# Kernel optimization log

Hardware: AMD Instinct MI355X
Metric: run time of the kernel (lower is better)

## Reference

```python
import jax, jax.numpy as jnp
import numpy as np

C = 64          # residual channels
N_LAYERS = 30
MAX_STEPS = 200
SQRT2 = 2.0 ** 0.5


def _conv1d(x, W, b, dilation=1, pad=0):
    # x: [B, Cin, T], W: [Cout, Cin, K], b: [Cout]
    y = jax.lax.conv_general_dilated(
        x, W, window_strides=(1,), padding=[(pad, pad)],
        rhs_dilation=(dilation,), dimension_numbers=('NCH', 'OIH', 'NCH'))
    return y + b[None, :, None]


def _silu(x):
    return x * jax.nn.sigmoid(x)


def _emb_table():
    steps = jnp.arange(MAX_STEPS, dtype=jnp.float32)[:, None]      # [200,1]
    dims = jnp.arange(64, dtype=jnp.float32)[None, :]              # [1,64]
    t = steps * 10.0 ** (dims * 4.0 / 63.0)                        # [200,64]
    return jnp.concatenate([jnp.sin(t), jnp.cos(t)], axis=1)       # [200,128]


def setup_inputs() -> dict:
    key = jax.random.key(0)
    ks = jax.random.split(key, 20)
    B, T = 4, 16384
    f32 = jnp.float32
    inp = {
        'audio': jax.random.normal(ks[0], (B, 1, T), dtype=f32),
        'diffusion_step': jax.random.randint(ks[1], (B,), 0, MAX_STEPS),
        # input projection Conv1d(1, 64, 1)
        'in_W': jax.random.normal(ks[2], (C, 1, 1), f32) * 1.0,
        'in_b': jax.random.normal(ks[3], (C,), f32) * 0.01,
        # diffusion embedding MLP 128->512->512
        'p1_W': jax.random.normal(ks[4], (512, 128), f32) * (1.0 / np.sqrt(128)),
        'p1_b': jnp.zeros((512,), f32),
        'p2_W': jax.random.normal(ks[5], (512, 512), f32) * (1.0 / np.sqrt(512)),
        'p2_b': jnp.zeros((512,), f32),
        # per-layer params (stacked over 30 layers)
        'dw_W': jax.random.normal(ks[6], (N_LAYERS, 2 * C, C, 3), f32) * (1.0 / np.sqrt(3 * C)),
        'dw_b': jnp.zeros((N_LAYERS, 2 * C), f32),
        'dp_W': jax.random.normal(ks[7], (N_LAYERS, C, 512), f32) * (1.0 / np.sqrt(512)),
        'dp_b': jnp.zeros((N_LAYERS, C), f32),
        'op_W': jax.random.normal(ks[8], (N_LAYERS, 2 * C, C, 1), f32) * (1.0 / np.sqrt(C)),
        'op_b': jnp.zeros((N_LAYERS, 2 * C), f32),
        # skip projection Conv1d(64,64,1)
        'sk_W': jax.random.normal(ks[9], (C, C, 1), f32) * (1.0 / np.sqrt(C)),
        'sk_b': jnp.zeros((C,), f32),
        # output projection Conv1d(64,1,1), weight zero-init like original
        'out_W': jnp.zeros((1, C, 1), f32),
        'out_b': jax.random.normal(ks[10], (1,), f32) * 0.01,
    }
    return inp


def reference(audio, diffusion_step, in_W, in_b, p1_W, p1_b, p2_W, p2_b,
              dw_W, dw_b, dp_W, dp_b, op_W, op_b, sk_W, sk_b, out_W, out_b):
    x = jax.nn.relu(_conv1d(audio, in_W, in_b))                    # [B,64,T]
    # diffusion embedding
    t = _emb_table()[diffusion_step]                               # [B,128]
    t = _silu(t @ p1_W.T + p1_b)                                   # [B,512]
    t = _silu(t @ p2_W.T + p2_b)                                   # [B,512]
    skip = None
    for i in range(N_LAYERS):
        d = 2 ** (i % 10)
        cond = (t @ dp_W[i].T + dp_b[i])[:, :, None]               # [B,64,1]
        y = _conv1d(x + cond, dw_W[i], dw_b[i], dilation=d, pad=d) # [B,128,T]
        gate, filt = y[:, :C], y[:, C:]
        y = jax.nn.sigmoid(gate) * jnp.tanh(filt)                  # [B,64,T]
        y = _conv1d(y, op_W[i], op_b[i])                           # [B,128,T]
        residual, sk = y[:, :C], y[:, C:]
        x = (x + residual) / SQRT2
        skip = sk if skip is None else skip + sk
    x = skip / np.sqrt(float(N_LAYERS)).astype(np.float32)
    x = jax.nn.relu(_conv1d(x, sk_W, sk_b))
    return _conv1d(x, out_W, out_b)                                # [B,1,T]
```

## Files before the change

### kernel.cpp

```cpp
#include <hip/hip_runtime.h>
#include <math.h>

#define C 64
#define NL 30
#define T 16384
#define B 4

typedef __bf16 bf16_t;
typedef __bf16 bf16x8 __attribute__((ext_vector_type(8)));
typedef __bf16 bf16x4 __attribute__((ext_vector_type(4)));
typedef float f32x4 __attribute__((ext_vector_type(4)));

typedef const __attribute__((address_space(1))) unsigned int glb_u32;
typedef __attribute__((address_space(3))) unsigned int lds_u32;

constexpr float INV_SQRT2   = 0.70710678118654752440f;
constexpr float INV_SQRT_NL = 0.18257418583505537115f;

__device__ __forceinline__ float fsig(float x) {
    return __builtin_amdgcn_rcpf(1.f + __builtin_amdgcn_exp2f(-1.44269504089f * x));
}
__device__ __forceinline__ float ftanh(float x) {
    return fmaf(2.f, __builtin_amdgcn_rcpf(1.f + __builtin_amdgcn_exp2f(-2.88539008178f * x)), -1.f);
}
__device__ __forceinline__ int swz(int off) { return off ^ ((off >> 3) & 0x70); }

__global__ void pack_weights(const float* __restrict__ dw_W,
                             const float* __restrict__ op_W,
                             const float* __restrict__ sk_W,
                             bf16_t* __restrict__ convpk,
                             bf16_t* __restrict__ oppk,
                             bf16_t* __restrict__ skpk) {
    int idx = blockIdx.x * 256 + threadIdx.x;
    const int ndw = NL * 128 * 192;
    const int nop = NL * 128 * 64;
    if (idx < ndw) {
        int k = idx % 192; int r = idx / 192;
        int oc = r % 128;  int l = r / 128;
        int tap = k >> 6, ic = k & 63;
        convpk[idx] = (bf16_t)dw_W[((l * 128 + oc) * 64 + ic) * 3 + tap];
    } else if (idx < ndw + nop) {
        oppk[idx - ndw] = (bf16_t)op_W[idx - ndw];
    } else if (idx < ndw + nop + 4096) {
        int j = idx - ndw - nop;
        skpk[j] = (bf16_t)(sk_W[j] * INV_SQRT_NL);
    }
}

__global__ void cond_embp1(const int* __restrict__ step,
                           const float* __restrict__ p1_W, const float* __restrict__ p1_b,
                           float* __restrict__ h1out) {
    __shared__ float e[128];
    __shared__ float red[256];
    int b = blockIdx.x, blk = blockIdx.y, tid = threadIdx.x;
    int s = step[b];
    if (tid < 128) {
        int d = tid & 63;
        float tf = (float)s * powf(10.f, (float)d * 4.f / 63.f);
        double td = (double)tf;
        e[tid] = (tid < 64) ? (float)sin(td) : (float)cos(td);
    }
    __syncthreads();
    int ol = tid >> 2, q = tid & 3;
    int o = blk * 64 + ol;
    const float4* wr = (const float4*)(p1_W + o * 128 + q * 32);
    const float4* ev = (const float4*)(e + q * 32);
    float a = 0.f;
    #pragma unroll
    for (int j = 0; j < 8; ++j) {
        float4 wv = wr[j]; float4 xv = ev[j];
        a = fmaf(wv.x, xv.x, a); a = fmaf(wv.y, xv.y, a);
        a = fmaf(wv.z, xv.z, a); a = fmaf(wv.w, xv.w, a);
    }
    red[tid] = a;
    __syncthreads();
    if (q == 0) {
        float v = red[tid] + red[tid + 1] + red[tid + 2] + red[tid + 3] + p1_b[o];
        h1out[b * 512 + o] = v / (1.f + expf(-v));
    }
}

__global__ void cond_p2(const float* __restrict__ h1,
                        const float* __restrict__ p2_W, const float* __restrict__ p2_b,
                        float* __restrict__ h2out) {
    __shared__ float red[256];
    int b = blockIdx.x, blk = blockIdx.y, tid = threadIdx.x;
    int ol = tid >> 2, q = tid & 3;
    int o = blk * 64 + ol;
    const float4* wr = (const float4*)(p2_W + o * 512 + q * 128);
    const float4* hv = (const float4*)(h1 + b * 512 + q * 128);
    float a = 0.f;
    #pragma unroll 8
    for (int j = 0; j < 32; ++j) {
        float4 wv = wr[j]; float4 xv = hv[j];
        a = fmaf(wv.x, xv.x, a); a = fmaf(wv.y, xv.y, a);
        a = fmaf(wv.z, xv.z, a); a = fmaf(wv.w, xv.w, a);
    }
    red[tid] = a;
    __syncthreads();
    if (q == 0) {
        float v = red[tid] + red[tid + 1] + red[tid + 2] + red[tid + 3] + p2_b[o];
        h2out[b * 512 + o] = v / (1.f + expf(-v));
    }
}

__global__ void cond_stage2b(const float* __restrict__ h2,
                             const float* __restrict__ dp_W, const float* __restrict__ dp_b,
                             const bf16_t* __restrict__ convpk,
                             const float* __restrict__ dw_b,
                             float* __restrict__ bias2) {
    __shared__ float red[256];
    __shared__ float cond_s[64];
    int l = blockIdx.x, b = blockIdx.y;
    int tid = threadIdx.x;
    {
        int o = tid >> 2, q = tid & 3;
        const float4* wr = (const float4*)(dp_W + ((size_t)l * C + o) * 512 + q * 128);
        const float4* h = (const float4*)(h2 + b * 512 + q * 128);
        float a = 0.f;
        #pragma unroll 8
        for (int j = 0; j < 32; ++j) {
            float4 wv = wr[j]; float4 hv = h[j];
            a = fmaf(wv.x, hv.x, a); a = fmaf(wv.y, hv.y, a);
            a = fmaf(wv.z, hv.z, a); a = fmaf(wv.w, hv.w, a);
        }
        red[tid] = a;
        __syncthreads();
        if (q == 0)
            cond_s[o] = red[tid] + red[tid + 1] + red[tid + 2] + red[tid + 3] + dp_b[l * C + o];
    }
    __syncthreads();
    int oc = tid & 127, kh = tid >> 7;
    const bf16_t* wr = convpk + ((size_t)l * 128 + oc) * 192 + kh * 96;
    float a = kh ? 0.f : dw_b[l * 128 + oc];
    #pragma unroll
    for (int j = 0; j < 96; ++j)
        a = fmaf((float)wr[j], cond_s[(kh * 96 + j) & 63], a);
    __syncthreads();
    red[tid] = a;
    __syncthreads();
    if (tid < 128)
        bias2[(l * B + b) * 128 + tid] = red[tid] + red[tid + 128];
}

__global__ void in_conv(const float* __restrict__ audio,
                        const float* __restrict__ in_W, const float* __restrict__ in_b,
                        bf16_t* __restrict__ x) {
    int idx = blockIdx.x * 256 + threadIdx.x;
    int cb = idx & 7;
    int t = (idx >> 3) & (T - 1);
    int b = idx >> 17;
    float av = audio[b * T + t];
    bf16x8 o;
    #pragma unroll
    for (int j = 0; j < 8; ++j) {
        int c = cb * 8 + j;
        o[j] = (bf16_t)fmaxf(fmaf(in_W[c], av, in_b[c]), 0.f);
    }
    *(bf16x8*)(x + ((size_t)b * T + t) * 64 + cb * 8) = o;
}

__global__ __launch_bounds__(256) void layer_kernel(
    const bf16_t* __restrict__ x_in, bf16_t* __restrict__ x_out, bf16_t* __restrict__ skip,
    const bf16_t* __restrict__ convpk, const bf16_t* __restrict__ oppk,
    const float* __restrict__ bias2, const float* __restrict__ op_b,
    const bf16_t* __restrict__ zpage,
    int layer, int dil, int first)
{
    __shared__ uint4 smem_u[4096];
    char* sm = (char*)smem_u;

    int tid = threadIdx.x;
    int w = __builtin_amdgcn_readfirstlane(tid >> 6);
    int l = tid & 63;
    int lr = l & 15;
    int g = l >> 4;
    int b = blockIdx.y;
    int tbase = blockIdx.x * 128;
    const bf16_t* xb = x_in + (size_t)b * T * 64;
    const bool m1 = (dil <= 32);

#define STAGE_M1(Sbase, t0s, R)                                              \
    _Pragma("unroll")                                                        \
    for (int r = 0; r < (R); ++r) {                                          \
        int q = r * 4096 + tid * 16;                                         \
        int row = q >> 7, c16 = (q >> 4) & 7;                                \
        int ts = (t0s) - dil + row;                                          \
        int c16s = c16 ^ (row & 7);                                          \
        const bf16_t* src = ((unsigned)ts < (unsigned)T)                     \
            ? xb + (size_t)ts * 64 + c16s * 8 : zpage + c16s * 8;            \
        __builtin_amdgcn_global_load_lds((glb_u32*)src,                      \
            (lds_u32*)(sm + (Sbase) + r * 4096 + w * 1024), 16, 0, 0);       \
    }
#define STAGE_M3(Sbase, t0s)                                                 \
    _Pragma("unroll")                                                        \
    for (int it = 0; it < 6; ++it) {                                         \
        int qq = it * 256 + tid;                                             \
        int slice = qq >> 9, row = (qq >> 3) & 63, c16 = qq & 7;             \
        int ts = (t0s) + row + (slice - 1) * dil;                            \
        int c16s = c16 ^ (row & 7);                                          \
        const bf16_t* src = ((unsigned)ts < (unsigned)T)                     \
            ? xb + (size_t)ts * 64 + c16s * 8 : zpage + c16s * 8;            \
        __builtin_amdgcn_global_load_lds((glb_u32*)src,                      \
            (lds_u32*)(sm + (Sbase) + it * 4096 + w * 1024), 16, 0, 0);      \
    }

    if (dil <= 16) {
        STAGE_M1(0, tbase, 3)
        STAGE_M1(24576, tbase + 64, 3)
        asm volatile("s_waitcnt vmcnt(3)" ::: "memory");
    } else if (dil == 32) {
        STAGE_M1(0, tbase, 4)
        STAGE_M1(24576, tbase + 64, 4)
        asm volatile("s_waitcnt vmcnt(4)" ::: "memory");
    } else {
        STAGE_M3(0, tbase)
        STAGE_M3(24576, tbase + 64)
        asm volatile("s_waitcnt vmcnt(6)" ::: "memory");
    }
    __builtin_amdgcn_s_barrier();
    __builtin_amdgcn_sched_barrier(0);
    asm volatile("" ::: "memory");

    bf16x8 cA[2][6];
    const bf16_t* cw = convpk + (size_t)layer * 128 * 192;
    #pragma unroll
    for (int mf = 0; mf < 2; ++mf)
        #pragma unroll
        for (int kf = 0; kf < 6; ++kf)
            cA[mf][kf] = *(const bf16x8*)(cw + (mf * 64 + w * 16 + lr) * 192 + kf * 32 + g * 8);
    bf16x8 oA[2][2];
    const bf16_t* ow = oppk + (size_t)layer * 128 * 64;
    #pragma unroll
    for (int mf = 0; mf < 2; ++mf)
        #pragma unroll
        for (int kf = 0; kf < 2; ++kf)
            oA[mf][kf] = *(const bf16x8*)(ow + (mf * 64 + w * 16 + lr) * 64 + kf * 32 + g * 8);
    f32x4 bC[2], bO[2];
    const float* b2 = bias2 + (layer * B + b) * 128;
    const float* ob = op_b + layer * 2 * C;
    #pragma unroll
    for (int mf = 0; mf < 2; ++mf)
        #pragma unroll
        for (int r = 0; r < 4; ++r) {
            bC[mf][r] = b2[mf * 64 + w * 16 + g * 4 + r];
            bO[mf][r] = ob[mf * 64 + w * 16 + g * 4 + r];
        }

    size_t bb = (size_t)b * T * 64;
    int tapstride = m1 ? dil * 128 : 8192;
    int t1off = m1 ? dil * 128 : 8192;

    for (int st = 0; st < 2; ++st) {
        int Sb = st * 24576;
        int zb = 49152 + st * 8192;
        int t0 = tbase + st * 64;

        f32x4 acc[2][4];
        #pragma unroll
        for (int mf = 0; mf < 2; ++mf)
            #pragma unroll
            for (int nf = 0; nf < 4; ++nf) acc[mf][nf] = bC[mf];
        #pragma unroll
        for (int kf = 0; kf < 6; ++kf) {
            int tap = kf >> 1;
            int kc = (kf & 1) * 32;
            bf16x8 Bf[4];
            #pragma unroll
            for (int nf = 0; nf < 4; ++nf) {
                int off = Sb + tap * tapstride + (nf * 16 + lr) * 128 + (kc + g * 8) * 2;
                Bf[nf] = *(const bf16x8*)(sm + swz(off));
            }
            #pragma unroll
            for (int mf = 0; mf < 2; ++mf)
                #pragma unroll
                for (int nf = 0; nf < 4; ++nf)
                    acc[mf][nf] = __builtin_amdgcn_mfma_f32_16x16x32_bf16(
                        cA[mf][kf], Bf[nf], acc[mf][nf], 0, 0, 0);
        }

        #pragma unroll
        for (int nf = 0; nf < 4; ++nf) {
            union { bf16_t hh[4]; uint2 u; } zp;
            #pragma unroll
            for (int r = 0; r < 4; ++r)
                zp.hh[r] = (bf16_t)(fsig(acc[0][nf][r]) * ftanh(acc[1][nf][r]));
            int off = zb + (nf * 16 + lr) * 128 + (w * 16 + g * 4) * 2;
            *(uint2*)(sm + swz(off)) = zp.u;
        }
        __syncthreads();

        f32x4 acc2[2][4];
        #pragma unroll
        for (int mf = 0; mf < 2; ++mf)
            #pragma unroll
            for (int nf = 0; nf < 4; ++nf) acc2[mf][nf] = bO[mf];
        #pragma unroll
        for (int kf = 0; kf < 2; ++kf) {
            bf16x8 Zf[4];
            #pragma unroll
            for (int nf = 0; nf < 4; ++nf) {
                int off = zb + (nf * 16 + lr) * 128 + (kf * 32 + g * 8) * 2;
                Zf[nf] = *(const bf16x8*)(sm + swz(off));
            }
            #pragma unroll
            for (int mf = 0; mf < 2; ++mf)
                #pragma unroll
                for (int nf = 0; nf < 4; ++nf)
                    acc2[mf][nf] = __builtin_amdgcn_mfma_f32_16x16x32_bf16(
                        oA[mf][kf], Zf[nf], acc2[mf][nf], 0, 0, 0);
        }

        #pragma unroll
        for (int nf = 0; nf < 4; ++nf) {
            int t = t0 + nf * 16 + lr;
            int c0 = w * 16 + g * 4;
            int xoff = Sb + t1off + (nf * 16 + lr) * 128 + c0 * 2;
            bf16x4 xv = *(const bf16x4*)(sm + swz(xoff));
            bf16x4 ro, so;
            bf16_t* sp = skip + bb + (size_t)t * 64 + c0;
            if (first) {
                #pragma unroll
                for (int r = 0; r < 4; ++r) {
                    ro[r] = (bf16_t)(((float)xv[r] + acc2[0][nf][r]) * INV_SQRT2);
                    so[r] = (bf16_t)acc2[1][nf][r];
                }
            } else {
                bf16x4 sv = *(const bf16x4*)sp;
                #pragma unroll
                for (int r = 0; r < 4; ++r) {
                    ro[r] = (bf16_t)(((float)xv[r] + acc2[0][nf][r]) * INV_SQRT2);
                    so[r] = (bf16_t)((float)sv[r] + acc2[1][nf][r]);
                }
            }
            *(bf16x4*)(x_out + bb + (size_t)t * 64 + c0) = ro;
            *(bf16x4*)sp = so;
        }
    }
#undef STAGE_M1
#undef STAGE_M3
}

__global__ __launch_bounds__(256) void final_kernel(
    const bf16_t* __restrict__ skip, const bf16_t* __restrict__ skpk,
    const float* __restrict__ sk_b,
    const float* __restrict__ out_W, const float* __restrict__ out_b,
    float* __restrict__ out)
{
    __shared__ uint4 tile_u[512];
    __shared__ float part[16][66];
    unsigned char* sm = (unsigned char*)tile_u;
    int tid = threadIdx.x;
    int w = __builtin_amdgcn_readfirstlane(tid >> 6);
    int l = tid & 63, lr = l & 15, g = l >> 4;
    int b = blockIdx.y, t0 = blockIdx.x * 64;
    const bf16_t* sb = skip + (size_t)b * T * 64;

    #pragma unroll
    for (int it = 0; it < 2; ++it) {
        int q = it * 256 + tid;
        int row = q >> 3, c16 = q & 7;
        uint4 val = *(const uint4*)(sb + (size_t)(t0 + row) * 64 + c16 * 8);
        *(uint4*)(sm + swz(row * 128 + c16 * 16)) = val;
    }

    bf16x8 aS[2];
    #pragma unroll
    for (int kf = 0; kf < 2; ++kf)
        aS[kf] = *(const bf16x8*)(skpk + (w * 16 + lr) * 64 + kf * 32 + g * 8);
    f32x4 acc[4];
    #pragma unroll
    for (int nf = 0; nf < 4; ++nf)
        #pragma unroll
        for (int r = 0; r < 4; ++r) acc[nf][r] = sk_b[w * 16 + g * 4 + r];
    __syncthreads();

    #pragma unroll
    for (int kf = 0; kf < 2; ++kf) {
        bf16x8 Bf[4];
        #pragma unroll
        for (int nf = 0; nf < 4; ++nf) {
            int off = (nf * 16 + lr) * 128 + (kf * 32 + g * 8) * 2;
            Bf[nf] = *(const bf16x8*)(sm + swz(off));
        }
        #pragma unroll
        for (int nf = 0; nf < 4; ++nf)
            acc[nf] = __builtin_amdgcn_mfma_f32_16x16x32_bf16(aS[kf], Bf[nf], acc[nf], 0, 0, 0);
    }

    #pragma unroll
    for (int nf = 0; nf < 4; ++nf) {
        float o = 0.f;
        #pragma unroll
        for (int r = 0; r < 4; ++r)
            o = fmaf(out_W[w * 16 + g * 4 + r], fmaxf(acc[nf][r], 0.f), o);
        part[w * 4 + g][nf * 16 + lr] = o;
    }
    __syncthreads();
    if (tid < 64) {
        float o = out_b[0];
        #pragma unroll
        for (int j = 0; j < 16; ++j) o += part[j][tid];
        out[(size_t)b * T + t0 + tid] = o;
    }
}

extern "C" void kernel_launch(void* const* d_in, const int* in_sizes, int n_in,
                              void* d_out, int out_size, void* d_ws, size_t ws_size,
                              hipStream_t stream) {
    const float* audio = (const float*)d_in[0];
    const int*   dstep = (const int*)d_in[1];
    const float* in_W  = (const float*)d_in[2];
    const float* in_b  = (const float*)d_in[3];
    const float* p1_W  = (const float*)d_in[4];
    const float* p1_b  = (const float*)d_in[5];
    const float* p2_W  = (const float*)d_in[6];
    const float* p2_b  = (const float*)d_in[7];
    const float* dw_W  = (const float*)d_in[8];
    const float* dw_b  = (const float*)d_in[9];
    const float* dp_W  = (const float*)d_in[10];
    const float* dp_b  = (const float*)d_in[11];
    const float* op_W  = (const float*)d_in[12];
    const float* op_b  = (const float*)d_in[13];
    const float* sk_W  = (const float*)d_in[14];
    const float* sk_b  = (const float*)d_in[15];
    const float* out_W = (const float*)d_in[16];
    const float* out_b = (const float*)d_in[17];

    float* ws = (float*)d_ws;
    const size_t NXE = (size_t)B * T * 64;
    float* h1    = ws;
    float* h2    = h1 + B * 512;
    float* bias2 = h2 + B * 512;
    float* zpg   = bias2 + NL * B * 128;
    bf16_t* xA   = (bf16_t*)(zpg + 128);
    bf16_t* xB   = xA + NXE;
    bf16_t* skip = xB + NXE;
    bf16_t* convpk = skip + NXE;
    bf16_t* oppk   = convpk + (size_t)NL * 128 * 192;
    bf16_t* skpk   = oppk + (size_t)NL * 128 * 64;

    hipMemsetAsync(zpg, 0, 512, stream);
    hipLaunchKernelGGL(pack_weights, dim3(3856), dim3(256), 0, stream,
                       dw_W, op_W, sk_W, convpk, oppk, skpk);
    hipLaunchKernelGGL(cond_embp1, dim3(B, 8), dim3(256), 0, stream,
                       dstep, p1_W, p1_b, h1);
    hipLaunchKernelGGL(cond_p2, dim3(B, 8), dim3(256), 0, stream,
                       h1, p2_W, p2_b, h2);
    hipLaunchKernelGGL(cond_stage2b, dim3(NL, B), dim3(256), 0, stream,
                       h2, dp_W, dp_b, convpk, dw_b, bias2);
    hipLaunchKernelGGL(in_conv, dim3(B * T * 8 / 256), dim3(256), 0, stream,
                       audio, in_W, in_b, xA);
    for (int i = 0; i < NL; ++i) {
        bf16_t* xin  = (i & 1) ? xB : xA;
        bf16_t* xout = (i & 1) ? xA : xB;
        int dil = 1 << (i % 10);
        hipLaunchKernelGGL(layer_kernel, dim3(T / 128, B), dim3(256), 0, stream,
                           xin, xout, skip, convpk, oppk, bias2, op_b,
                           (const bf16_t*)zpg, i, dil, (i == 0) ? 1 : 0);
    }
    hipLaunchKernelGGL(final_kernel, dim3(T / 64, B), dim3(256), 0, stream,
                       skip, skpk, sk_b, out_W, out_b, (float*)d_out);
}
```

Baseline: 514.1 us.

## Shrink layer kernel LDS via dynamic shared memory sized per dilation

Switches the layer kernel from a fixed 64KB static LDS buffer to dynamic shared memory sized per dilation (32–40KB). For small dilations the two 64-step slabs are packed tightly, and for large dilations (64+) a single 3-tap slab is restaged per sub-tile with extra barriers instead of staging both up front. The aim is to fit more workgroups per CU, trading away some load/compute overlap in the large-dilation layers.

```diff
diff --git a/kernel.cpp b/kernel.cpp
--- a/kernel.cpp
+++ b/kernel.cpp
@@ -167,8 +167,7 @@
     const bf16_t* __restrict__ zpage,
     int layer, int dil, int first)
 {
-    __shared__ uint4 smem_u[4096];
-    char* sm = (char*)smem_u;
+    extern __shared__ char sm[];
 
     int tid = threadIdx.x;
     int w = __builtin_amdgcn_readfirstlane(tid >> 6);
@@ -178,13 +177,13 @@
     int b = blockIdx.y;
     int tbase = blockIdx.x * 128;
     const bf16_t* xb = x_in + (size_t)b * T * 64;
-    const bool m1 = (dil <= 32);
-
-#define STAGE_M1(Sbase, t0s, R)                                              \
+    const bool dual = (dil <= 32);
+    const int R = (dil <= 16) ? 3 : 4;
+
+#define STAGE_SLAB(Sbase, t0s, RR)                                           \
     _Pragma("unroll")                                                        \
-    for (int r = 0; r < (R); ++r) {                                          \
-        int q = r * 4096 + tid * 16;                                         \
-        int row = q >> 7, c16 = (q >> 4) & 7;                                \
+    for (int r = 0; r < (RR); ++r) {                                         \
+        int row = r * 32 + (tid >> 3), c16 = tid & 7;                        \
         int ts = (t0s) - dil + row;                                          \
         int c16s = c16 ^ (row & 7);                                          \
         const bf16_t* src = ((unsigned)ts < (unsigned)T)                     \
@@ -192,7 +191,7 @@
         __builtin_amdgcn_global_load_lds((glb_u32*)src,                      \
             (lds_u32*)(sm + (Sbase) + r * 4096 + w * 1024), 16, 0, 0);       \
     }
-#define STAGE_M3(Sbase, t0s)                                                 \
+#define STAGE_M3(t0s)                                                        \
     _Pragma("unroll")                                                        \
     for (int it = 0; it < 6; ++it) {                                         \
         int qq = it * 256 + tid;                                             \
@@ -202,25 +201,22 @@
         const bf16_t* src = ((unsigned)ts < (unsigned)T)                     \
             ? xb + (size_t)ts * 64 + c16s * 8 : zpage + c16s * 8;            \
         __builtin_amdgcn_global_load_lds((glb_u32*)src,                      \
-            (lds_u32*)(sm + (Sbase) + it * 4096 + w * 1024), 16, 0, 0);      \
-    }
-
-    if (dil <= 16) {
-        STAGE_M1(0, tbase, 3)
-        STAGE_M1(24576, tbase + 64, 3)
-        asm volatile("s_waitcnt vmcnt(3)" ::: "memory");
-    } else if (dil == 32) {
-        STAGE_M1(0, tbase, 4)
-        STAGE_M1(24576, tbase + 64, 4)
-        asm volatile("s_waitcnt vmcnt(4)" ::: "memory");
-    } else {
-        STAGE_M3(0, tbase)
-        STAGE_M3(24576, tbase + 64)
-        asm volatile("s_waitcnt vmcnt(6)" ::: "memory");
-    }
-    __builtin_amdgcn_s_barrier();
-    __builtin_amdgcn_sched_barrier(0);
-    asm volatile("" ::: "memory");
+            (lds_u32*)(sm + it * 4096 + w * 1024), 16, 0, 0);                \
+    }
+
+    if (dual) {
+        if (dil <= 16) {
+            STAGE_SLAB(0, tbase, 3)
+            STAGE_SLAB(12288, tbase + 64, 3)
+            asm volatile("s_waitcnt vmcnt(3)" ::: "memory");
+        } else {
+            STAGE_SLAB(0, tbase, 4)
+            STAGE_SLAB(16384, tbase + 64, 4)
+            asm volatile("s_waitcnt vmcnt(4)" ::: "memory");
+        }
+        __builtin_amdgcn_s_barrier();
+        __builtin_amdgcn_sched_barrier(0);
+    }
 
     bf16x8 cA[2][6];
     const bf16_t* cw = convpk + (size_t)layer * 128 * 192;
@@ -248,13 +244,17 @@
         }
 
     size_t bb = (size_t)b * T * 64;
-    int tapstride = m1 ? dil * 128 : 8192;
-    int t1off = m1 ? dil * 128 : 8192;
+    const int zb = dual ? 2 * R * 4096 : 24576;
+    const int tapstride = dual ? dil * 128 : 8192;
 
     for (int st = 0; st < 2; ++st) {
-        int Sb = st * 24576;
-        int zb = 49152 + st * 8192;
+        int Sb = dual ? st * R * 4096 : 0;
         int t0 = tbase + st * 64;
+
+        if (!dual) {
+            STAGE_M3(t0)
+            __syncthreads();
+        }
 
         f32x4 acc[2][4];
         #pragma unroll
@@ -315,7 +315,7 @@
         for (int nf = 0; nf < 4; ++nf) {
             int t = t0 + nf * 16 + lr;
             int c0 = w * 16 + g * 4;
-            int xoff = Sb + t1off + (nf * 16 + lr) * 128 + c0 * 2;
+            int xoff = Sb + tapstride + (nf * 16 + lr) * 128 + c0 * 2;
             bf16x4 xv = *(const bf16x4*)(sm + swz(xoff));
             bf16x4 ro, so;
             bf16_t* sp = skip + bb + (size_t)t * 64 + c0;
@@ -336,8 +336,9 @@
             *(bf16x4*)(x_out + bb + (size_t)t * 64 + c0) = ro;
             *(bf16x4*)sp = so;
         }
-    }
-#undef STAGE_M1
+        if (st == 0) __syncthreads();
+    }
+#undef STAGE_SLAB
 #undef STAGE_M3
 }
 
@@ -455,7 +456,8 @@
         bf16_t* xin  = (i & 1) ? xB : xA;
         bf16_t* xout = (i & 1) ? xA : xB;
         int dil = 1 << (i % 10);
-        hipLaunchKernelGGL(layer_kernel, dim3(T / 128, B), dim3(256), 0, stream,
+        int shmem = (dil <= 16) ? 32768 : (dil <= 32 ? 40960 : 32768);
+        hipLaunchKernelGGL(layer_kernel, dim3(T / 128, B), dim3(256), shmem, stream,
                            xin, xout, skip, convpk, oppk, bias2, op_b,
                            (const bf16_t*)zpg, i, dil, (i == 0) ? 1 : 0);
     }
```

Result: faster. 499.5 us (-2.9%).
